# Kernel optimization log

Measured on AMD Instinct MI355X. Metric: run time of the kernel, lower is better.

Reference implementation:

```python
import jax, jax.numpy as jnp
import numpy as np

B, S, D, H = 4, 1024, 1024, 16
DH = D // H
LN_EPS = 1e-5


def setup_inputs() -> dict:
    key = jax.random.key(0)
    ks = jax.random.split(key, 12)
    lim = 1.0 / np.sqrt(D)
    u = lambda k, shp: jax.random.uniform(k, shp, jnp.float32, -lim, lim)
    return {
        "x": jax.random.normal(ks[0], (B, S, D), jnp.float32),
        "Wq": u(ks[1], (D, D)), "bq": u(ks[2], (D,)),
        "Wk": u(ks[3], (D, D)), "bk": u(ks[4], (D,)),
        "Wv": u(ks[5], (D, D)), "bv": u(ks[6], (D,)),
        "Wo": u(ks[7], (D, D)), "bo": u(ks[8], (D,)),
        "gamma": jnp.ones((D,), jnp.float32),
        "beta": jnp.zeros((D,), jnp.float32),
    }


def _layer_norm(x, gamma, beta):
    mu = jnp.mean(x, axis=-1, keepdims=True)
    var = jnp.mean(jnp.square(x - mu), axis=-1, keepdims=True)
    return (x - mu) * jax.lax.rsqrt(var + LN_EPS) * gamma + beta


def reference(x, Wq, bq, Wk, bk, Wv, bv, Wo, bo, gamma, beta):
    # Linear projections (torch Linear: x @ W^T + b)
    Q = x @ Wq.T + bq  # [B, S, D]
    K = x @ Wk.T + bk
    V = x @ Wv.T + bv
    # Faithful to original: raw view(B*H, S, DH) with NO head transpose
    Q = Q.reshape(B * H, S, DH)
    K = K.reshape(B * H, S, DH)
    V = V.reshape(B * H, S, DH)
    scale = DH ** -0.5
    attn = jnp.einsum('bqd,bkd->bqk', Q, K) * scale  # [B*H, S, S]
    attn = jax.nn.softmax(attn, axis=-1)
    ctx = jnp.einsum('bqk,bkd->bqd', attn, V)  # [B*H, S, DH]
    ctx = ctx.reshape(B, S, D)
    out = ctx @ Wo.T + bo
    out = out + x  # residual (dropout p=0.0 is identity)
    return _layer_norm(out, gamma, beta)
```

## Files before the change

kernel.cpp:

```cpp
#include <hip/hip_runtime.h>
#include <hip/hip_bf16.h>


using u16 = unsigned short;
typedef __attribute__((ext_vector_type(8))) short bf16x8;
typedef __attribute__((ext_vector_type(4))) float f32x4;
typedef __attribute__((ext_vector_type(4))) u16  u16x4;
typedef __attribute__((ext_vector_type(8))) u16  u16x8;

#define AS1C(p) ((const __attribute__((address_space(1))) void*)(p))
#define AS3(p)  ((__attribute__((address_space(3))) void*)(p))

__device__ __forceinline__ u16 f2bf(float f) {
  union { float f; unsigned u; } v; v.f = f;
  unsigned u = v.u;
  return (u16)((u + 0x7fffu + ((u >> 16) & 1u)) >> 16);
}

__device__ __forceinline__ f32x4 mfma16(bf16x8 a, bf16x8 b, f32x4 c) {
  return __builtin_amdgcn_mfma_f32_16x16x32_bf16(a, b, c, 0, 0, 0);
}

__global__ __launch_bounds__(256) void prep_kernel(
    const float* __restrict__ x,
    const float* __restrict__ wq, const float* __restrict__ wk,
    const float* __restrict__ wv, const float* __restrict__ wo,
    const float* __restrict__ bq, const float* __restrict__ bk, const float* __restrict__ bv,
    u16* __restrict__ xb, u16* __restrict__ wb, float* __restrict__ bc)
{
  int ch = blockIdx.x * 256 + threadIdx.x;
  if (ch < 2097152) {
    const float* src; u16* dst;
    if (ch < 1048576) { src = x + ch * 4; dst = xb + ch * 4; }
    else {
      int c2 = ch - 1048576;
      int wsel = c2 >> 18;
      int off  = c2 & 262143;
      const float* wsrc[4] = { wq, wk, wv, wo };
      src = wsrc[wsel] + off * 4;
      dst = wb + wsel * 1048576 + off * 4;
    }
    f32x4 v = *(const f32x4*)src;
    u16x4 o;
    o[0] = f2bf(v[0]); o[1] = f2bf(v[1]); o[2] = f2bf(v[2]); o[3] = f2bf(v[3]);
    *(u16x4*)dst = o;
  } else {
    int c3 = ch - 2097152;
    int bsel = c3 >> 8, off = c3 & 255;
    const float* bsrc[3] = { bq, bk, bv };
    f32x4 v = *(const f32x4*)(bsrc[bsel] + off * 4);
    *(f32x4*)(bc + bsel * 1024 + off * 4) = v;
  }
}

template <int MODE>
__global__ __launch_bounds__(256) void gemm_bt(
    const u16* __restrict__ A, const u16* __restrict__ Bw,
    const float* __restrict__ bias, const float* __restrict__ resid,
    u16* __restrict__ outb, float* __restrict__ outf)
{
  __shared__ u16 As[2][4096];
  __shared__ u16 Bs[2][4096];
  const int K = 1024;
  int bm = blockIdx.x, bn = blockIdx.y;
  int tid = threadIdx.x;
  int wid = tid >> 6, lane = tid & 63;
  int g = lane >> 4, lr = lane & 15;
  int wr = wid >> 1, wc = wid & 1;

  f32x4 acc[4][4] = {};

  int sch  = (tid >> 6) * 64 + (tid & 63);
  int srow = tid >> 2, skp = tid & 3;
  const u16* gaBase = A  + (size_t)(bm * 128 + srow) * K + skp * 8;
  const u16* gbBase = Bw + (size_t)(bn * 128 + srow) * K + skp * 8;
  int srow2 = 64 + srow;
  const u16* gaBase2 = A  + (size_t)(bm * 128 + srow2) * K + skp * 8;
  const u16* gbBase2 = Bw + (size_t)(bn * 128 + srow2) * K + skp * 8;

#define STAGE_GEMM(b, kt) do { \
    __builtin_amdgcn_global_load_lds(AS1C(gaBase  + (kt) * 32), AS3(&As[b][tid * 8]),        16, 0, 0); \
    __builtin_amdgcn_global_load_lds(AS1C(gbBase  + (kt) * 32), AS3(&Bs[b][tid * 8]),        16, 0, 0); \
    __builtin_amdgcn_global_load_lds(AS1C(gaBase2 + (kt) * 32), AS3(&As[b][2048 + tid * 8]), 16, 0, 0); \
    __builtin_amdgcn_global_load_lds(AS1C(gbBase2 + (kt) * 32), AS3(&Bs[b][2048 + tid * 8]), 16, 0, 0); \
  } while (0)

  STAGE_GEMM(0, 0);
  __syncthreads();
  int cur = 0;

  for (int kt = 0; kt < K / 32; ++kt) {
    if (kt + 1 < K / 32) STAGE_GEMM(cur ^ 1, kt + 1);

    bf16x8 af[4], bfr[4];
#pragma unroll
    for (int m = 0; m < 4; ++m)
      af[m] = *(const bf16x8*)&As[cur][(wr * 64 + m * 16 + lr) * 32 + 8 * g];
#pragma unroll
    for (int n = 0; n < 4; ++n)
      bfr[n] = *(const bf16x8*)&Bs[cur][(wc * 64 + n * 16 + lr) * 32 + 8 * g];
#pragma unroll
    for (int m = 0; m < 4; ++m)
#pragma unroll
      for (int n = 0; n < 4; ++n)
        acc[m][n] = mfma16(af[m], bfr[n], acc[m][n]);
    __syncthreads();
    cur ^= 1;
  }

#pragma unroll
  for (int m = 0; m < 4; ++m) {
    int row0 = bm * 128 + wr * 64 + m * 16 + 4 * g;
#pragma unroll
    for (int n = 0; n < 4; ++n) {
      int col = bn * 128 + wc * 64 + n * 16 + lr;
#pragma unroll
      for (int i = 0; i < 4; ++i) {
        float v = acc[m][n][i];
        if (MODE == 0) {
          v += bias[col];
          int r = row0 + i;
          if (col < 1024) {
            outb[(size_t)r * 1024 + col] = f2bf(v * 0.125f);
          } else if (col < 2048) {
            outb[4194304 + (size_t)r * 1024 + (col - 1024)] = f2bf(v);
          } else {
            int c = col - 2048;
            outb[8388608 + (size_t)(r >> 6) * 65536 + (size_t)(c & 63) * 1024
                 + (r & 63) * 16 + (c >> 6)] = f2bf(v);
          }
        } else {
          size_t idx = (size_t)(row0 + i) * 1024 + col;
          outf[idx] = v + bias[col] + resid[idx];
        }
      }
    }
  }
}

__global__ __launch_bounds__(512) void attn_kernel(
    const u16* __restrict__ Qb, const u16* __restrict__ Kb,
    const u16* __restrict__ Vtb, u16* __restrict__ Ob)
{
  __shared__ u16 Ks[2][64 * 64];
  __shared__ u16 Vts[2][64 * 64];
  __shared__ u16 Ps[8][16 * 72];

  int blk = blockIdx.x;
  int bh = blk & 63, qt = blk >> 6;
  int tid = threadIdx.x, wid = tid >> 6, lane = tid & 63;
  int g = lane >> 4, lr = lane & 15;

  const u16* Qp = Qb  + (size_t)bh * 65536;
  const u16* Kp = Kb  + (size_t)bh * 65536;
  const u16* Vp = Vtb + (size_t)bh * 65536;

  bf16x8 qf[2];
#pragma unroll
  for (int f = 0; f < 2; ++f)
    qf[f] = *(const bf16x8*)&Qp[(size_t)(qt * 128 + wid * 16 + lr) * 64 + f * 32 + 8 * g];

  f32x4 oacc[4] = {};
  float mrow[4], lrowv[4];
#pragma unroll
  for (int i = 0; i < 4; ++i) { mrow[i] = -1e30f; lrowv[i] = 0.f; }

  int kc  = tid >> 3, scc = tid & 7;
  const u16* gkBase = Kp + (size_t)kc * 64 + (size_t)(scc ^ (kc & 7)) * 8;
  const u16* gvBase = Vp + (size_t)kc * 1024 + (size_t)(scc ^ (kc & 7)) * 8;

#define STAGE_ATTN(b, kt) do { \
    __builtin_amdgcn_global_load_lds(AS1C(gkBase + (size_t)(kt) * 4096), AS3(&Ks[b][tid * 8]),  16, 0, 0); \
    __builtin_amdgcn_global_load_lds(AS1C(gvBase + (kt) * 64),           AS3(&Vts[b][tid * 8]), 16, 0, 0); \
  } while (0)

  STAGE_ATTN(0, 0);
  __syncthreads();
  int cur = 0;

  for (int kt = 0; kt < 16; ++kt) {
    if (kt + 1 < 16) STAGE_ATTN(cur ^ 1, kt + 1);

    f32x4 s[4];
#pragma unroll
    for (int n = 0; n < 4; ++n) {
      f32x4 z = { 0.f, 0.f, 0.f, 0.f };
      int kr = n * 16 + lr;
#pragma unroll
      for (int f = 0; f < 2; ++f) {
        bf16x8 kb = *(const bf16x8*)&Ks[cur][kr * 64 + (((f * 4 + g) ^ (kr & 7)) * 8)];
        z = mfma16(qf[f], kb, z);
      }
      s[n] = z;
    }

    float corr[4], pvv[4][4];
#pragma unroll
    for (int i = 0; i < 4; ++i) {
      float tm = fmaxf(fmaxf(s[0][i], s[1][i]), fmaxf(s[2][i], s[3][i]));
#pragma unroll
      for (int ms = 1; ms < 16; ms <<= 1) tm = fmaxf(tm, __shfl_xor(tm, ms));
      float mn = fmaxf(mrow[i], tm);
      corr[i] = __expf(mrow[i] - mn);
      float rs = 0.f;
#pragma unroll
      for (int n = 0; n < 4; ++n) {
        float p = __expf(s[n][i] - mn);
        pvv[n][i] = p; rs += p;
      }
#pragma unroll
      for (int ms = 1; ms < 16; ms <<= 1) rs += __shfl_xor(rs, ms);
      lrowv[i] = lrowv[i] * corr[i] + rs;
      mrow[i] = mn;
    }
#pragma unroll
    for (int nd = 0; nd < 4; ++nd) {
      f32x4 o = oacc[nd];
      o[0] *= corr[0]; o[1] *= corr[1]; o[2] *= corr[2]; o[3] *= corr[3];
      oacc[nd] = o;
    }

#pragma unroll
    for (int n = 0; n < 4; ++n)
#pragma unroll
      for (int i = 0; i < 4; ++i)
        Ps[wid][(4 * g + i) * 72 + n * 16 + lr] = f2bf(pvv[n][i]);
    asm volatile("s_waitcnt lgkmcnt(0)" ::: "memory");

#pragma unroll
    for (int f = 0; f < 2; ++f) {
      bf16x8 pa = *(const bf16x8*)&Ps[wid][lr * 72 + f * 32 + 8 * g];
#pragma unroll
      for (int nd = 0; nd < 4; ++nd) {
        int dr = nd * 16 + lr;
        bf16x8 vb = *(const bf16x8*)&Vts[cur][dr * 64 + (((f * 4 + g) ^ (dr & 7)) * 8)];
        oacc[nd] = mfma16(pa, vb, oacc[nd]);
      }
    }
    __syncthreads();
    cur ^= 1;
  }

  u16* Op = Ob + (size_t)bh * 65536 + (size_t)(qt * 128 + wid * 16) * 64;
#pragma unroll
  for (int nd = 0; nd < 4; ++nd)
#pragma unroll
    for (int i = 0; i < 4; ++i)
      Op[(4 * g + i) * 64 + nd * 16 + lr] = f2bf(oacc[nd][i] / lrowv[i]);
}

__global__ __launch_bounds__(256) void ln_kernel(
    float* __restrict__ out, const float* __restrict__ gamma, const float* __restrict__ beta)
{
  int row = blockIdx.x, tid = threadIdx.x;
  int lane = tid & 63, wid = tid >> 6;
  f32x4 v = *(const f32x4*)&out[(size_t)row * 1024 + tid * 4];
  float s = v[0] + v[1] + v[2] + v[3];
  float q = v[0] * v[0] + v[1] * v[1] + v[2] * v[2] + v[3] * v[3];
#pragma unroll
  for (int ms = 1; ms < 64; ms <<= 1) { s += __shfl_xor(s, ms); q += __shfl_xor(q, ms); }
  __shared__ float red[8];
  if (lane == 0) { red[wid] = s; red[wid + 4] = q; }
  __syncthreads();
  s = red[0] + red[1] + red[2] + red[3];
  q = red[4] + red[5] + red[6] + red[7];
  float mu = s * (1.f / 1024.f);
  float var = q * (1.f / 1024.f) - mu * mu;
  float inv = rsqrtf(var + 1e-5f);
  f32x4 g4 = *(const f32x4*)&gamma[tid * 4];
  f32x4 b4 = *(const f32x4*)&beta[tid * 4];
  f32x4 o;
#pragma unroll
  for (int j = 0; j < 4; ++j) o[j] = (v[j] - mu) * inv * g4[j] + b4[j];
  *(f32x4*)&out[(size_t)row * 1024 + tid * 4] = o;
}

extern "C" void kernel_launch(void* const* d_in, const int* in_sizes, int n_in,
                              void* d_out, int out_size, void* d_ws, size_t ws_size,
                              hipStream_t stream) {
  const float* x     = (const float*)d_in[0];
  const float* Wq    = (const float*)d_in[1];
  const float* bq    = (const float*)d_in[2];
  const float* Wk    = (const float*)d_in[3];
  const float* bk    = (const float*)d_in[4];
  const float* Wv    = (const float*)d_in[5];
  const float* bv    = (const float*)d_in[6];
  const float* Wo    = (const float*)d_in[7];
  const float* bo    = (const float*)d_in[8];
  const float* gamma = (const float*)d_in[9];
  const float* beta  = (const float*)d_in[10];
  float* out = (float*)d_out;

  char* ws = (char*)d_ws;
  u16*   xb  = (u16*)ws;
  u16*   wb  = (u16*)(ws + (8u << 20));
  float* bc  = (float*)(ws + (16u << 20));
  u16*   qkv = (u16*)(ws + (16u << 20) + 16384);
  u16*   ctx = xb;

  prep_kernel<<<8195, 256, 0, stream>>>(x, Wq, Wk, Wv, Wo, bq, bk, bv, xb, wb, bc);

  dim3 g0(32, 24);
  gemm_bt<0><<<g0, 256, 0, stream>>>(xb, wb, bc, nullptr, qkv, nullptr);

  attn_kernel<<<512, 512, 0, stream>>>(qkv, qkv + 4194304, qkv + 8388608, ctx);

  dim3 g1(32, 8);
  gemm_bt<1><<<g1, 256, 0, stream>>>(ctx, wb + 3 * 1048576, bo, x, nullptr, out);

  ln_kernel<<<4096, 256, 0, stream>>>(out, gamma, beta);
}
```

Baseline: 150.4 us.

## Rewrite GEMMs with 4-stage LDS pipeline, XOR swizzle, and XCD-aware block mapping

Replaces the double-buffered GEMM with a templated kernel that prefetches three K-tiles ahead into four LDS buffers, using explicit vmcnt waits and barriers. It adds an XOR swizzle on the LDS chunk layout to avoid bank conflicts and remaps block IDs so that neighbouring tiles land on the same XCD. It also raises the MFMA issue priority. The QKV projection now uses 256x256 tiles with 8 waves. The trade-offs are more LDS per block, which lowers occupancy, and fewer blocks (192) for the QKV GEMM.

Measured after the change: 187.1 us. 24.5% more time.

```diff
diff --git a/kernel.cpp b/kernel.cpp
--- a/kernel.cpp
+++ b/kernel.cpp
@@ -53,67 +53,112 @@
   }
 }
 
-template <int MODE>
-__global__ __launch_bounds__(256) void gemm_bt(
+template <int BT, int NWAVE, int MODE, int GM>
+__global__ __launch_bounds__(NWAVE * 64) void gemm_tpl(
     const u16* __restrict__ A, const u16* __restrict__ Bw,
     const float* __restrict__ bias, const float* __restrict__ resid,
     u16* __restrict__ outb, float* __restrict__ outf)
 {
-  __shared__ u16 As[2][4096];
-  __shared__ u16 Bs[2][4096];
+  constexpr int MREP = BT / 32;
+  constexpr int NREP = 4;
+  constexpr int WN = NWAVE / 2;
+  constexpr int TE = BT * 32;
+  __shared__ u16 As[4][TE];
+  __shared__ u16 Bs[4][TE];
+
   const int K = 1024;
-  int bm = blockIdx.x, bn = blockIdx.y;
-  int tid = threadIdx.x;
-  int wid = tid >> 6, lane = tid & 63;
+  int tid = threadIdx.x, w = tid >> 6, lane = tid & 63;
   int g = lane >> 4, lr = lane & 15;
-  int wr = wid >> 1, wc = wid & 1;
-
-  f32x4 acc[4][4] = {};
-
-  int sch  = (tid >> 6) * 64 + (tid & 63);
-  int srow = tid >> 2, skp = tid & 3;
-  const u16* gaBase = A  + (size_t)(bm * 128 + srow) * K + skp * 8;
-  const u16* gbBase = Bw + (size_t)(bn * 128 + srow) * K + skp * 8;
-  int srow2 = 64 + srow;
-  const u16* gaBase2 = A  + (size_t)(bm * 128 + srow2) * K + skp * 8;
-  const u16* gbBase2 = Bw + (size_t)(bn * 128 + srow2) * K + skp * 8;
-
-#define STAGE_GEMM(b, kt) do { \
-    __builtin_amdgcn_global_load_lds(AS1C(gaBase  + (kt) * 32), AS3(&As[b][tid * 8]),        16, 0, 0); \
-    __builtin_amdgcn_global_load_lds(AS1C(gbBase  + (kt) * 32), AS3(&Bs[b][tid * 8]),        16, 0, 0); \
-    __builtin_amdgcn_global_load_lds(AS1C(gaBase2 + (kt) * 32), AS3(&As[b][2048 + tid * 8]), 16, 0, 0); \
-    __builtin_amdgcn_global_load_lds(AS1C(gbBase2 + (kt) * 32), AS3(&Bs[b][2048 + tid * 8]), 16, 0, 0); \
-  } while (0)
-
-  STAGE_GEMM(0, 0);
-  __syncthreads();
-  int cur = 0;
-
-  for (int kt = 0; kt < K / 32; ++kt) {
-    if (kt + 1 < K / 32) STAGE_GEMM(cur ^ 1, kt + 1);
-
-    bf16x8 af[4], bfr[4];
-#pragma unroll
-    for (int m = 0; m < 4; ++m)
-      af[m] = *(const bf16x8*)&As[cur][(wr * 64 + m * 16 + lr) * 32 + 8 * g];
-#pragma unroll
-    for (int n = 0; n < 4; ++n)
-      bfr[n] = *(const bf16x8*)&Bs[cur][(wc * 64 + n * 16 + lr) * 32 + 8 * g];
-#pragma unroll
-    for (int m = 0; m < 4; ++m)
-#pragma unroll
-      for (int n = 0; n < 4; ++n)
+  int wr = w / WN, wcn = w % WN;
+
+  int nwg = gridDim.x;
+  int cpx = nwg >> 3;
+  int bid = blockIdx.x;
+  int swz = (bid & 7) * cpx + (bid >> 3);
+  int bm = swz % GM, bn = swz / GM;
+
+  int ch0 = w * 64 + lane;
+  int ch1 = ch0 + NWAVE * 64;
+  auto srcoff = [&](int ch) -> size_t {
+    int r = ch >> 2, pc = ch & 3;
+    int gc = pc ^ ((r >> 2) & 3);
+    return (size_t)r * K + gc * 8;
+  };
+  const u16* aS0 = A  + (size_t)(bm * BT) * K + srcoff(ch0);
+  const u16* aS1 = A  + (size_t)(bm * BT) * K + srcoff(ch1);
+  const u16* bS0 = Bw + (size_t)(bn * BT) * K + srcoff(ch0);
+  const u16* bS1 = Bw + (size_t)(bn * BT) * K + srcoff(ch1);
+  int lo0 = ch0 * 8, lo1 = ch1 * 8;
+
+  auto STAGE = [&](int buf, int kt) {
+    __builtin_amdgcn_global_load_lds(AS1C(aS0 + kt * 32), AS3(&As[buf][lo0]), 16, 0, 0);
+    __builtin_amdgcn_global_load_lds(AS1C(aS1 + kt * 32), AS3(&As[buf][lo1]), 16, 0, 0);
+    __builtin_amdgcn_global_load_lds(AS1C(bS0 + kt * 32), AS3(&Bs[buf][lo0]), 16, 0, 0);
+    __builtin_amdgcn_global_load_lds(AS1C(bS1 + kt * 32), AS3(&Bs[buf][lo1]), 16, 0, 0);
+  };
+
+  f32x4 acc[MREP][NREP] = {};
+  int pc8 = (g ^ ((lr >> 2) & 3)) * 8;
+
+  auto COMPUTE = [&](int buf) {
+    bf16x8 af[MREP], bfr[NREP];
+#pragma unroll
+    for (int m = 0; m < MREP; ++m)
+      af[m] = *(const bf16x8*)&As[buf][(wr * (BT / 2) + m * 16 + lr) * 32 + pc8];
+#pragma unroll
+    for (int n = 0; n < NREP; ++n)
+      bfr[n] = *(const bf16x8*)&Bs[buf][(wcn * 64 + n * 16 + lr) * 32 + pc8];
+    __builtin_amdgcn_s_setprio(1);
+#pragma unroll
+    for (int m = 0; m < MREP; ++m)
+#pragma unroll
+      for (int n = 0; n < NREP; ++n)
         acc[m][n] = mfma16(af[m], bfr[n], acc[m][n]);
-    __syncthreads();
-    cur ^= 1;
+    __builtin_amdgcn_s_setprio(0);
+  };
+
+  STAGE(0, 0); STAGE(1, 1); STAGE(2, 2);
+
+#pragma unroll 4
+  for (int t = 0; t < 28; ++t) {
+    STAGE((t + 3) & 3, t + 3);
+    asm volatile("s_waitcnt vmcnt(12)" ::: "memory");
+    __builtin_amdgcn_sched_barrier(0);
+    __builtin_amdgcn_s_barrier();
+    COMPUTE(t & 3);
+    __builtin_amdgcn_s_barrier();
+    __builtin_amdgcn_sched_barrier(0);
   }
-
-#pragma unroll
-  for (int m = 0; m < 4; ++m) {
-    int row0 = bm * 128 + wr * 64 + m * 16 + 4 * g;
-#pragma unroll
-    for (int n = 0; n < 4; ++n) {
-      int col = bn * 128 + wc * 64 + n * 16 + lr;
+  STAGE(3, 31);
+  asm volatile("s_waitcnt vmcnt(12)" ::: "memory");
+  __builtin_amdgcn_sched_barrier(0);
+  __builtin_amdgcn_s_barrier();
+  COMPUTE(0);
+  __builtin_amdgcn_s_barrier();
+  __builtin_amdgcn_sched_barrier(0);
+  asm volatile("s_waitcnt vmcnt(8)" ::: "memory");
+  __builtin_amdgcn_sched_barrier(0);
+  __builtin_amdgcn_s_barrier();
+  COMPUTE(1);
+  __builtin_amdgcn_s_barrier();
+  __builtin_amdgcn_sched_barrier(0);
+  asm volatile("s_waitcnt vmcnt(4)" ::: "memory");
+  __builtin_amdgcn_sched_barrier(0);
+  __builtin_amdgcn_s_barrier();
+  COMPUTE(2);
+  __builtin_amdgcn_s_barrier();
+  __builtin_amdgcn_sched_barrier(0);
+  asm volatile("s_waitcnt vmcnt(0)" ::: "memory");
+  __builtin_amdgcn_sched_barrier(0);
+  __builtin_amdgcn_s_barrier();
+  COMPUTE(3);
+
+#pragma unroll
+  for (int m = 0; m < MREP; ++m) {
+    int row0 = bm * BT + wr * (BT / 2) + m * 16 + 4 * g;
+#pragma unroll
+    for (int n = 0; n < NREP; ++n) {
+      int col = bn * BT + wcn * 64 + n * 16 + lr;
 #pragma unroll
       for (int i = 0; i < 4; ++i) {
         float v = acc[m][n][i];
@@ -300,13 +345,11 @@
 
   prep_kernel<<<8195, 256, 0, stream>>>(x, Wq, Wk, Wv, Wo, bq, bk, bv, xb, wb, bc);
 
-  dim3 g0(32, 24);
-  gemm_bt<0><<<g0, 256, 0, stream>>>(xb, wb, bc, nullptr, qkv, nullptr);
+  gemm_tpl<256, 8, 0, 16><<<192, 512, 0, stream>>>(xb, wb, bc, nullptr, qkv, nullptr);
 
   attn_kernel<<<512, 512, 0, stream>>>(qkv, qkv + 4194304, qkv + 8388608, ctx);
 
-  dim3 g1(32, 8);
-  gemm_bt<1><<<g1, 256, 0, stream>>>(ctx, wb + 3 * 1048576, bo, x, nullptr, out);
+  gemm_tpl<128, 4, 1, 32><<<256, 256, 0, stream>>>(ctx, wb + 3 * 1048576, bo, x, nullptr, out);
 
   ln_kernel<<<4096, 256, 0, stream>>>(out, gamma, beta);
 }
```
